# Performance work log

Measured on AMD Instinct MI355X. Metric: run time of the kernel, lower is better.

Reference implementation:

```python
import jax, jax.numpy as jnp
import numpy as np


def setup_inputs() -> dict:
    key = jax.random.key(0)
    ks = jax.random.split(key, 6)
    B, N, D, E, S, H = 4, 4096, 768, 4, 1024, 3072
    sc = lambda d: 1.0 / np.sqrt(d)
    return {
        "x": jax.random.normal(ks[0], (B, N, D), dtype=jnp.float32),
        "phi": jax.random.normal(ks[1], (E, S, D), dtype=jnp.float32) * sc(D),
        "w1": jax.random.normal(ks[2], (E, D, H), dtype=jnp.float32) * sc(D),
        "b1": jnp.zeros((E, H), dtype=jnp.float32),
        "w2": jax.random.normal(ks[3], (E, H, D), dtype=jnp.float32) * sc(H),
        "b2": jnp.zeros((E, D), dtype=jnp.float32),
    }


def reference(x, phi, w1, b1, w2, b2):
    # x: [B,N,D], phi: [E,S,D]
    logits = jnp.einsum('bnd,esd->bnes', x, phi)          # [B,N,E,S]
    B, N, E, S = logits.shape
    dispatch = jax.nn.softmax(logits, axis=1)             # softmax over tokens
    combine = jax.nn.softmax(
        logits.reshape(B, N, E * S), axis=-1
    ).reshape(B, N, E, S)                                 # softmax over all slots
    slots = jnp.einsum('bnd,bnes->besd', x, dispatch)     # [B,E,S,D]
    h = jax.nn.gelu(jnp.einsum('besd,edh->besh', slots, w1) + b1[None, :, None, :])
    y = jnp.einsum('besh,ehd->besd', h, w2) + b2[None, :, None, :]
    out = jnp.einsum('besd,bnes->bnd', y, combine)        # [B,N,D]
    return out
```

## Files before the change

kernel.cpp:

```cpp
#include <hip/hip_runtime.h>
#include <hip/hip_bf16.h>

using u16 = unsigned short;
using short8 = __attribute__((ext_vector_type(8))) short;
using floatx4 = __attribute__((ext_vector_type(4))) float;

#define DEVI static __device__ __forceinline__

constexpr int cB = 4, cN = 4096, cD = 768, cE = 4, cS = 1024, cH = 3072;
constexpr int cES = cE * cS;
constexpr int cHC = cH / 2;

DEVI u16 f2bf(float f) {
  union { float f; unsigned u; } v; v.f = f;
  unsigned r = v.u + 0x7fffu + ((v.u >> 16) & 1u);
  return (u16)(r >> 16);
}
DEVI float bf2f(u16 b) {
  union { unsigned u; float f; } v; v.u = ((unsigned)b) << 16;
  return v.f;
}
DEVI float gelu_tanh(float x) {
  float z = 1.5957691216057308f * (x + 0.044715f * x * x * x);
  z = fminf(fmaxf(z, -30.f), 30.f);
  float e = __expf(z);
  float t = (e - 1.f) / (e + 1.f);
  return 0.5f * x * (1.f + t);
}

DEVI void glds16(const u16* g, u16* l) {
  __builtin_amdgcn_global_load_lds(
      (const __attribute__((address_space(1))) void*)g,
      (__attribute__((address_space(3))) void*)l, 16, 0, 0);
}

__global__ __launch_bounds__(256) void zero_kernel(float* __restrict__ p, int n) {
  int i = blockIdx.x * 256 + threadIdx.x;
  if (i < n) p[i] = 0.f;
}

__global__ __launch_bounds__(256) void convert_kernel(const float* __restrict__ in,
                                                      u16* __restrict__ out, long n) {
  long stride = (long)gridDim.x * 256 * 4;
  for (long idx = ((long)blockIdx.x * 256 + threadIdx.x) * 4; idx < n; idx += stride) {
    float4 v = *(const float4*)(in + idx);
    ushort4 o;
    o.x = f2bf(v.x); o.y = f2bf(v.y); o.z = f2bf(v.z); o.w = f2bf(v.w);
    *(ushort4*)(out + idx) = o;
  }
}

DEVI u16 to_bf(float f) { return f2bf(f); }
DEVI u16 to_bf(u16 u) { return u; }

template <typename Tin>
__global__ __launch_bounds__(256) void transpose_bf16_kernel(const Tin* __restrict__ in,
                                                             u16* __restrict__ out,
                                                             int R, int C,
                                                             long strideIn, long strideOut) {
  __shared__ u16 tile[64][65];
  const Tin* inb = in + (long)blockIdx.z * strideIn;
  u16* outb = out + (long)blockIdx.z * strideOut;
  const int r0 = blockIdx.y * 64, c0 = blockIdx.x * 64;
  const int tid = threadIdx.x;
#pragma unroll
  for (int i = 0; i < 16; i++) {
    int idx = i * 256 + tid;
    int r = idx >> 6, c = idx & 63;
    tile[r][c] = to_bf(inb[(long)(r0 + r) * C + (c0 + c)]);
  }
  __syncthreads();
#pragma unroll
  for (int i = 0; i < 16; i++) {
    int idx = i * 256 + tid;
    int r = idx >> 6, c = idx & 63;
    outb[(long)(c0 + r) * R + (r0 + c)] = tile[c][r];
  }
}

__global__ __launch_bounds__(256) void rowsum_kernel(const u16* __restrict__ P,
                                                     float* __restrict__ Z, int cols) {
  long base = (long)blockIdx.x * cols;
  int tid = threadIdx.x;
  float s = 0.f;
  for (int c = tid * 4; c < cols; c += 256 * 4) {
    ushort4 v = *(const ushort4*)(P + base + c);
    s += bf2f(v.x) + bf2f(v.y) + bf2f(v.z) + bf2f(v.w);
  }
  for (int o = 32; o > 0; o >>= 1) s += __shfl_down(s, o, 64);
  __shared__ float ws4[4];
  if ((tid & 63) == 0) ws4[tid >> 6] = s;
  __syncthreads();
  if (tid == 0) Z[blockIdx.x] = ws4[0] + ws4[1] + ws4[2] + ws4[3];
}

__global__ __launch_bounds__(256) void colsum_kernel(const u16* __restrict__ P,
                                                     float* __restrict__ Z, int cols) {
  int col = blockIdx.x * 256 + threadIdx.x;
  int r0 = blockIdx.y * 256;
  float s = 0.f;
  for (int r = r0; r < r0 + 256; r++) s += bf2f(P[(long)r * cols + col]);
  atomicAdd(Z + col, s);
}

template <int EPI>
__global__ __launch_bounds__(256, 2) void gemm_nt(const u16* __restrict__ A,
                                                  const u16* __restrict__ Bm,
                                                  void* __restrict__ Cout,
                                                  int M, int Nn, int K,
                                                  long ldA, long ldB, long ldC,
                                                  long strideA, long strideB, int modB,
                                                  long strideC,
                                                  const float* __restrict__ epiVec,
                                                  long epiStride, int epiMod) {
  __shared__ u16 lds[4 * 8192];

  const int gx = gridDim.x;
  const int nwg = gx * gridDim.y;
  int flat = blockIdx.y * gx + blockIdx.x;
  if ((nwg & 7) == 0) flat = (flat & 7) * (nwg >> 3) + (flat >> 3);
  const int bxs = flat % gx, bys = flat / gx;

  const int bz = blockIdx.z;
  const u16* Ab = A + (long)bz * strideA;
  const u16* Bb = Bm + (long)(bz % modB) * strideB;
  const float* ev = epiVec + (long)(bz % epiMod) * epiStride;
  const int tileM = bys * 128, tileN = bxs * 128;
  const int tid = threadIdx.x;
  const int wave = tid >> 6, lane = tid & 63;
  const int quad = lane >> 4, l16 = lane & 15;
  const int wm = (wave >> 1) * 64, wn = (wave & 1) * 64;

  const int swzk = (((lane & 3) ^ ((lane >> 3) & 3)) << 3);
  const int r0 = wave * 32 + (lane >> 2);
  const u16* aG0 = Ab + (long)(tileM + r0) * ldA + swzk;
  const u16* aG1 = Ab + (long)(tileM + r0 + 16) * ldA + swzk;
  const u16* bG0 = Bb + (long)(tileN + r0) * ldB + swzk;
  const u16* bG1 = Bb + (long)(tileN + r0 + 16) * ldB + swzk;
  const int ldsW = wave * 1024;

  const int NT = K >> 5;

  auto STAGE = [&](int tt) {
    u16* l = &lds[(tt & 3) * 8192];
    const long ko = (long)tt << 5;
    glds16(aG0 + ko, l + ldsW);
    glds16(aG1 + ko, l + ldsW + 512);
    glds16(bG0 + ko, l + 4096 + ldsW);
    glds16(bG1 + ko, l + 4096 + ldsW + 512);
  };

  floatx4 acc[4][4] = {};
  const int sread = ((quad ^ ((l16 >> 1) & 3)) << 3);

  STAGE(0);
  if (NT > 1) STAGE(1);
  if (NT > 2) STAGE(2);

  for (int t = 0; t < NT; t++) {
    asm volatile("s_barrier" ::: "memory");
    if (t + 3 < NT) STAGE(t + 3);
    const int ahead = NT - 1 - t;
    if (ahead >= 3)      asm volatile("s_waitcnt vmcnt(12)" ::: "memory");
    else if (ahead == 2) asm volatile("s_waitcnt vmcnt(8)" ::: "memory");
    else if (ahead == 1) asm volatile("s_waitcnt vmcnt(4)" ::: "memory");
    else                 asm volatile("s_waitcnt vmcnt(0)" ::: "memory");
    asm volatile("s_barrier" ::: "memory");

    const u16* As = &lds[(t & 3) * 8192];
    const u16* Bs = As + 4096;
    short8 af[4], bq[4];
#pragma unroll
    for (int i = 0; i < 4; i++)
      af[i] = *(const short8*)&As[(wm + i * 16 + l16) * 32 + sread];
#pragma unroll
    for (int j = 0; j < 4; j++)
      bq[j] = *(const short8*)&Bs[(wn + j * 16 + l16) * 32 + sread];
    __builtin_amdgcn_s_setprio(1);
#pragma unroll
    for (int i = 0; i < 4; i++)
#pragma unroll
      for (int j = 0; j < 4; j++)
        acc[i][j] = __builtin_amdgcn_mfma_f32_16x16x32_bf16(af[i], bq[j], acc[i][j], 0, 0, 0);
    __builtin_amdgcn_s_setprio(0);
  }

  const long cBase = (long)bz * strideC;
#pragma unroll
  for (int i = 0; i < 4; i++) {
#pragma unroll
    for (int r = 0; r < 4; r++) {
      const int row = tileM + wm + i * 16 + quad * 4 + r;
      float rscale = 1.f;
      if (EPI == 1 || EPI == 4) rscale = 1.f / ev[row];
#pragma unroll
      for (int j = 0; j < 4; j++) {
        const int col = tileN + wn + j * 16 + l16;
        float v = acc[i][j][r];
        const long cIdx = cBase + (long)row * ldC + col;
        if (EPI == 0) v = __expf(v);
        if (EPI == 1 || EPI == 4) v *= rscale;
        if (EPI == 2) v = gelu_tanh(v + ev[col]);
        if (EPI == 3) v = v + ev[col];
        if (EPI == 5) v = v + bf2f(((u16*)Cout)[cIdx]);
        if (EPI == 4)
          ((float*)Cout)[cIdx] = v;
        else
          ((u16*)Cout)[cIdx] = f2bf(v);
      }
    }
  }
}

extern "C" void kernel_launch(void* const* d_in, const int* in_sizes, int n_in,
                              void* d_out, int out_size, void* d_ws, size_t ws_size,
                              hipStream_t stream) {
  const float* x   = (const float*)d_in[0];
  const float* phi = (const float*)d_in[1];
  const float* w1  = (const float*)d_in[2];
  const float* b1  = (const float*)d_in[3];
  const float* w2  = (const float*)d_in[4];
  const float* b2  = (const float*)d_in[5];
  (void)in_sizes; (void)n_in; (void)out_size; (void)ws_size;
  float* out_f = (float*)d_out;

  char* ws = (char*)d_ws;
  size_t off = 0;
  auto carve = [&](size_t bytes) -> char* {
    char* p = ws + off;
    off += (bytes + 255) & ~(size_t)255;
    return p;
  };

  const size_t SZ_P = (size_t)cN * cES * 2;
  char* R1 = carve(2 * SZ_P);
  u16* Pb  = (u16*)R1;
  u16* Ptb = (u16*)(R1 + SZ_P);
  u16* Hc  = (u16*)R1;
  u16* P2  = (u16*)R1;
  u16* Xbf = (u16*)carve((size_t)cB * cN * cD * 2);
  char* R3 = carve((size_t)cB * cD * cN * 2);
  u16* Xt = (u16*)R3;
  u16* Yv = (u16*)R3;
  char* R4 = carve((size_t)cB * cES * cD * 2);
  u16* Slots = (u16*)R4;
  u16* Yt    = (u16*)R4;
  u16* Phibf = (u16*)carve((size_t)cES * cD * 2);
  u16* W1t = (u16*)carve((size_t)cE * cH * cD * 2);
  u16* W2t = (u16*)carve((size_t)cE * cD * cH * 2);
  float* Z1 = (float*)carve((size_t)cB * cES * 4);
  float* Z2 = (float*)carve((size_t)cB * cN * 4);

  convert_kernel<<<2048, 256, 0, stream>>>(x, Xbf, (long)cB * cN * cD);
  convert_kernel<<<1024, 256, 0, stream>>>(phi, Phibf, (long)cES * cD);
  transpose_bf16_kernel<float><<<dim3(cH / 64, cD / 64, cE), 256, 0, stream>>>(
      w1, W1t, cD, cH, (long)cD * cH, (long)cH * cD);
  transpose_bf16_kernel<float><<<dim3(cD / 64, cH / 64, cE), 256, 0, stream>>>(
      w2, W2t, cH, cD, (long)cH * cD, (long)cD * cH);
  transpose_bf16_kernel<float><<<dim3(cD / 64, cN / 64, cB), 256, 0, stream>>>(
      x, Xt, cN, cD, (long)cN * cD, (long)cD * cN);
  zero_kernel<<<(cB * cES) / 256, 256, 0, stream>>>(Z1, cB * cES);

  for (int b = 0; b < cB; b++) {
    const u16* Xb = Xbf + (long)b * cN * cD;
    gemm_nt<0><<<dim3(cES / 128, cN / 128, 1), 256, 0, stream>>>(
        Xb, Phibf, Pb, cN, cES, cD, cD, cD, cES,
        0L, 0L, 1, 0L, Z1, 0, 1);
    colsum_kernel<<<dim3(cES / 256, cN / 256, 1), 256, 0, stream>>>(
        Pb, Z1 + (long)b * cES, cES);
    rowsum_kernel<<<cN, 256, 0, stream>>>(Pb, Z2 + (long)b * cN, cES);
    transpose_bf16_kernel<u16><<<dim3(cES / 64, cN / 64, 1), 256, 0, stream>>>(
        Pb, Ptb, cN, cES, 0L, 0L);
    gemm_nt<1><<<dim3(cD / 128, cES / 128, 1), 256, 0, stream>>>(
        Ptb, Xt + (long)b * cD * cN, Slots + (long)b * cES * cD,
        cES, cD, cN, cN, cN, cD,
        0L, 0L, 1, 0L, Z1 + (long)b * cES, 0, 1);
  }

  for (int hc = 0; hc < 2; hc++) {
    const int h0 = hc * cHC;
    gemm_nt<2><<<dim3(cHC / 128, cS / 128, cB * cE), 256, 0, stream>>>(
        Slots, W1t + (long)h0 * cD, Hc, cS, cHC, cD, cD, cD, cHC,
        (long)cS * cD, (long)cH * cD, cE, (long)cS * cHC, b1 + h0, cH, cE);
    if (hc == 0)
      gemm_nt<3><<<dim3(cD / 128, cS / 128, cB * cE), 256, 0, stream>>>(
          Hc, W2t + h0, Yv, cS, cD, cHC, cHC, cH, cD,
          (long)cS * cHC, (long)cD * cH, cE, (long)cS * cD, b2, cD, cE);
    else
      gemm_nt<5><<<dim3(cD / 128, cS / 128, cB * cE), 256, 0, stream>>>(
          Hc, W2t + h0, Yv, cS, cD, cHC, cHC, cH, cD,
          (long)cS * cHC, (long)cD * cH, cE, (long)cS * cD, b2, cD, cE);
  }

  transpose_bf16_kernel<u16><<<dim3(cD / 64, cES / 64, cB), 256, 0, stream>>>(
      Yv, Yt, cES, cD, (long)cES * cD, (long)cD * cES);
  for (int bp = 0; bp < 2; bp++) {
    const u16* Xb = Xbf + (long)(bp * 2) * cN * cD;
    gemm_nt<0><<<dim3(cES / 128, cN / 128, 2), 256, 0, stream>>>(
        Xb, Phibf, P2, cN, cES, cD, cD, cD, cES,
        (long)cN * cD, 0L, 1, (long)cN * cES, Z1, 0, 1);
    gemm_nt<4><<<dim3(cD / 128, cN / 128, 2), 256, 0, stream>>>(
        P2, Yt + (long)(bp * 2) * cD * cES, out_f + (long)(bp * 2) * cN * cD,
        cN, cD, cES, cES, cES, cD,
        (long)cN * cES, (long)cD * cES, 2, (long)cN * cD,
        Z2 + (long)(bp * 2) * cN, cN, 2);
  }
}
```

Before: 1.244 ms.

## Add 256x256-tile 8-wave GEMM kernel with XCD-aware block remap

Adds a gemm256 kernel that computes 256x256 output tiles with 512 threads, split-K halves, double-buffered LDS loads staged between MFMA phases, and a block-index remap that groups blocks across the eight XCDs. The logits, W1 and W2 GEMMs now use it in place of the 128x128 gemm_nt, which should raise data reuse per loaded tile and cut global traffic. The cost is more registers and LDS per block (128 KB declared) and fewer blocks for the smaller GEMMs; for example the W2 GEMM gets a 3x4x16 grid, which can leave CUs underused.

```diff
diff --git a/kernel.cpp b/kernel.cpp
--- a/kernel.cpp
+++ b/kernel.cpp
@@ -197,6 +197,158 @@
       for (int j = 0; j < 4; j++) {
         const int col = tileN + wn + j * 16 + l16;
         float v = acc[i][j][r];
+        const long cIdx = cBase + (long)row * ldC + col;
+        if (EPI == 0) v = __expf(v);
+        if (EPI == 1 || EPI == 4) v *= rscale;
+        if (EPI == 2) v = gelu_tanh(v + ev[col]);
+        if (EPI == 3) v = v + ev[col];
+        if (EPI == 5) v = v + bf2f(((u16*)Cout)[cIdx]);
+        if (EPI == 4)
+          ((float*)Cout)[cIdx] = v;
+        else
+          ((u16*)Cout)[cIdx] = f2bf(v);
+      }
+    }
+  }
+}
+
+template <int EPI>
+__global__ __launch_bounds__(512, 2) void gemm256(const u16* __restrict__ A,
+                                                  const u16* __restrict__ Bm,
+                                                  void* __restrict__ Cout,
+                                                  int M, int Nn, int K,
+                                                  long ldA, long ldB, long ldC,
+                                                  long strideA, long strideB, int modB,
+                                                  long strideC,
+                                                  const float* __restrict__ epiVec,
+                                                  long epiStride, int epiMod) {
+  __shared__ u16 lds[2][2][2][8192];
+
+  const int gx = gridDim.x;
+  const int nwg = gx * gridDim.y;
+  int flat = blockIdx.y * gx + blockIdx.x;
+  {
+    const int q = nwg >> 3, r = nwg & 7, xc = flat & 7, o = flat >> 3;
+    flat = (xc < r ? xc * (q + 1) : r * (q + 1) + (xc - r) * q) + o;
+  }
+  const int bxs = flat % gx, bys = flat / gx;
+
+  const int bz = blockIdx.z;
+  const u16* __restrict__ Ab = A + (long)bz * strideA;
+  const u16* __restrict__ Bb = Bm + (long)(bz % modB) * strideB;
+  const float* __restrict__ ev = epiVec + (long)(bz % epiMod) * epiStride;
+  const int tileM = bys * 256, tileN = bxs * 256;
+  const int tid = threadIdx.x;
+  const int wave = tid >> 6, lane = tid & 63;
+  const int quad = lane >> 4, l16 = lane & 15;
+  const int wr = wave >> 2, wc = wave & 3;
+
+  const int kswz = (((lane & 3) ^ ((lane >> 3) & 3)) << 3);
+  const int srow = wave * 32 + (lane >> 2);
+  const u16* gA = Ab + (long)(tileM + srow) * ldA + kswz;
+  const u16* gB = Bb + (long)(tileN + srow) * ldB + kswz;
+
+  const int rdsw = ((quad ^ ((l16 >> 1) & 3)) << 3);
+  const int aOff = (wr * 128 + l16) * 32 + rdsw;
+  const int bOff = (wc * 64 + l16) * 32 + rdsw;
+
+  const int NT = K >> 6;
+
+#define STA256(buf, kh, tt) do {                                   \
+    const u16* _g = gA + ((long)(tt) << 6) + ((kh) << 5);          \
+    u16* _l = &lds[buf][0][kh][wave * 1024];                       \
+    glds16(_g, _l); glds16(_g + 16 * ldA, _l + 512); } while (0)
+#define STB256(buf, kh, tt) do {                                   \
+    const u16* _g = gB + ((long)(tt) << 6) + ((kh) << 5);          \
+    u16* _l = &lds[buf][1][kh][wave * 1024];                       \
+    glds16(_g, _l); glds16(_g + 16 * ldB, _l + 512); } while (0)
+#define BAR256 asm volatile("s_barrier" ::: "memory")
+#define LGK0   asm volatile("s_waitcnt lgkmcnt(0)" ::: "memory")
+
+  floatx4 acc[8][4] = {};
+  short8 af[4], bq[4];
+
+  STA256(0, 0, 0); STB256(0, 0, 0); STA256(0, 1, 0); STB256(0, 1, 0);
+  STB256(1, 0, 1); STA256(1, 0, 1); STB256(1, 1, 1);
+  asm volatile("s_waitcnt vmcnt(6)" ::: "memory");
+  BAR256;
+
+#define TILE256(kt, buf) do {                                                      \
+    const bool s1 = (kt) + 1 < NT, s2 = (kt) + 2 < NT;                             \
+                                            \
+    _Pragma("unroll") for (int i = 0; i < 4; i++)                                  \
+      af[i] = *(const short8*)&lds[buf][0][0][aOff + i * 512];                     \
+    _Pragma("unroll") for (int n = 0; n < 4; n++)                                  \
+      bq[n] = *(const short8*)&lds[buf][1][0][bOff + n * 512];                     \
+    if (s1) STA256((buf) ^ 1, 1, (kt) + 1);                                        \
+    BAR256; LGK0;                                                                  \
+    __builtin_amdgcn_s_setprio(1);                                                 \
+    _Pragma("unroll") for (int i = 0; i < 4; i++)                                  \
+      _Pragma("unroll") for (int n = 0; n < 4; n++)                                \
+        acc[i][n] = __builtin_amdgcn_mfma_f32_16x16x32_bf16(af[i], bq[n], acc[i][n], 0, 0, 0); \
+    __builtin_amdgcn_s_setprio(0);                                                 \
+    BAR256;                                                                        \
+                                         \
+    _Pragma("unroll") for (int i = 0; i < 4; i++)                                  \
+      af[i] = *(const short8*)&lds[buf][0][0][aOff + (4 + i) * 512];               \
+    if (s2) STB256(buf, 0, (kt) + 2);                                              \
+    BAR256; LGK0;                                                                  \
+    __builtin_amdgcn_s_setprio(1);                                                 \
+    _Pragma("unroll") for (int i = 0; i < 4; i++)                                  \
+      _Pragma("unroll") for (int n = 0; n < 4; n++)                                \
+        acc[4 + i][n] = __builtin_amdgcn_mfma_f32_16x16x32_bf16(af[i], bq[n], acc[4 + i][n], 0, 0, 0); \
+    __builtin_amdgcn_s_setprio(0);                                                 \
+    BAR256;                                                                        \
+                                            \
+    _Pragma("unroll") for (int i = 0; i < 4; i++)                                  \
+      af[i] = *(const short8*)&lds[buf][0][1][aOff + i * 512];                     \
+    _Pragma("unroll") for (int n = 0; n < 4; n++)                                  \
+      bq[n] = *(const short8*)&lds[buf][1][1][bOff + n * 512];                     \
+    if (s2) STA256(buf, 0, (kt) + 2);                                              \
+    BAR256; LGK0;                                                                  \
+    __builtin_amdgcn_s_setprio(1);                                                 \
+    _Pragma("unroll") for (int i = 0; i < 4; i++)                                  \
+      _Pragma("unroll") for (int n = 0; n < 4; n++)                                \
+        acc[i][n] = __builtin_amdgcn_mfma_f32_16x16x32_bf16(af[i], bq[n], acc[i][n], 0, 0, 0); \
+    __builtin_amdgcn_s_setprio(0);                                                 \
+    BAR256;                                                                        \
+                                                    \
+    _Pragma("unroll") for (int i = 0; i < 4; i++)                                  \
+      af[i] = *(const short8*)&lds[buf][0][1][aOff + (4 + i) * 512];               \
+    if (s2) STB256(buf, 1, (kt) + 2);                                              \
+    BAR256; LGK0;                                                                  \
+    __builtin_amdgcn_s_setprio(1);                                                 \
+    _Pragma("unroll") for (int i = 0; i < 4; i++)                                  \
+      _Pragma("unroll") for (int n = 0; n < 4; n++)                                \
+        acc[4 + i][n] = __builtin_amdgcn_mfma_f32_16x16x32_bf16(af[i], bq[n], acc[4 + i][n], 0, 0, 0); \
+    __builtin_amdgcn_s_setprio(0);                                                 \
+    if (s2)      asm volatile("s_waitcnt vmcnt(6)" ::: "memory");                  \
+    else if (s1) asm volatile("s_waitcnt vmcnt(0)" ::: "memory");                  \
+    BAR256;                                                                        \
+  } while (0)
+
+  for (int kt = 0; kt < NT; kt += 2) {
+    TILE256(kt, 0);
+    TILE256(kt + 1, 1);
+  }
+#undef TILE256
+#undef STA256
+#undef STB256
+#undef BAR256
+#undef LGK0
+
+  const long cBase = (long)bz * strideC;
+#pragma unroll
+  for (int m = 0; m < 8; m++) {
+#pragma unroll
+    for (int r = 0; r < 4; r++) {
+      const int row = tileM + wr * 128 + m * 16 + quad * 4 + r;
+      float rscale = 1.f;
+      if (EPI == 1 || EPI == 4) rscale = 1.f / ev[row];
+#pragma unroll
+      for (int n = 0; n < 4; n++) {
+        const int col = tileN + wc * 64 + n * 16 + l16;
+        float v = acc[m][n][r];
         const long cIdx = cBase + (long)row * ldC + col;
         if (EPI == 0) v = __expf(v);
         if (EPI == 1 || EPI == 4) v *= rscale;
@@ -263,7 +415,7 @@
 
   for (int b = 0; b < cB; b++) {
     const u16* Xb = Xbf + (long)b * cN * cD;
-    gemm_nt<0><<<dim3(cES / 128, cN / 128, 1), 256, 0, stream>>>(
+    gemm256<0><<<dim3(cES / 256, cN / 256, 1), 512, 0, stream>>>(
         Xb, Phibf, Pb, cN, cES, cD, cD, cD, cES,
         0L, 0L, 1, 0L, Z1, 0, 1);
     colsum_kernel<<<dim3(cES / 256, cN / 256, 1), 256, 0, stream>>>(
@@ -279,15 +431,15 @@
 
   for (int hc = 0; hc < 2; hc++) {
     const int h0 = hc * cHC;
-    gemm_nt<2><<<dim3(cHC / 128, cS / 128, cB * cE), 256, 0, stream>>>(
+    gemm256<2><<<dim3(cHC / 256, cS / 256, cB * cE), 512, 0, stream>>>(
         Slots, W1t + (long)h0 * cD, Hc, cS, cHC, cD, cD, cD, cHC,
         (long)cS * cD, (long)cH * cD, cE, (long)cS * cHC, b1 + h0, cH, cE);
     if (hc == 0)
-      gemm_nt<3><<<dim3(cD / 128, cS / 128, cB * cE), 256, 0, stream>>>(
+      gemm256<3><<<dim3(cD / 256, cS / 256, cB * cE), 512, 0, stream>>>(
           Hc, W2t + h0, Yv, cS, cD, cHC, cHC, cH, cD,
           (long)cS * cHC, (long)cD * cH, cE, (long)cS * cD, b2, cD, cE);
     else
-      gemm_nt<5><<<dim3(cD / 128, cS / 128, cB * cE), 256, 0, stream>>>(
+      gemm256<5><<<dim3(cD / 256, cS / 256, cB * cE), 512, 0, stream>>>(
           Hc, W2t + h0, Yv, cS, cD, cHC, cHC, cH, cD,
           (long)cS * cHC, (long)cD * cH, cE, (long)cS * cD, b2, cD, cE);
   }
@@ -296,7 +448,7 @@
       Yv, Yt, cES, cD, (long)cES * cD, (long)cD * cES);
   for (int bp = 0; bp < 2; bp++) {
     const u16* Xb = Xbf + (long)(bp * 2) * cN * cD;
-    gemm_nt<0><<<dim3(cES / 128, cN / 128, 2), 256, 0, stream>>>(
+    gemm256<0><<<dim3(cES / 256, cN / 256, 2), 512, 0, stream>>>(
         Xb, Phibf, P2, cN, cES, cD, cD, cD, cES,
         (long)cN * cD, 0L, 1, (long)cN * cES, Z1, 0, 1);
     gemm_nt<4><<<dim3(cD / 128, cN / 128, 2), 256, 0, stream>>>(
```

After: 1.169 ms. 1.06x faster.
